# Kernel optimization log

Measured on AMD Instinct MI355X. Metric: run time of the kernel, lower is better.

Reference implementation:

```python
import jax, jax.numpy as jnp
import numpy as np

D_MODEL = 1024
NHEAD = 16
D_HEAD = D_MODEL // NHEAD


def setup_inputs() -> dict:
    key = jax.random.key(0)
    ks = jax.random.split(key, 9)
    B, S = 2, 2048
    scale = 1.0 / np.sqrt(D_MODEL)
    x = jax.random.normal(ks[0], (B, S, D_MODEL), dtype=jnp.float32)
    Wq = jax.random.normal(ks[1], (D_MODEL, D_MODEL), dtype=jnp.float32) * scale
    Wk = jax.random.normal(ks[2], (D_MODEL, D_MODEL), dtype=jnp.float32) * scale
    Wv = jax.random.normal(ks[3], (D_MODEL, D_MODEL), dtype=jnp.float32) * scale
    Wo = jax.random.normal(ks[4], (D_MODEL, D_MODEL), dtype=jnp.float32) * scale
    bq = jax.random.normal(ks[5], (D_MODEL,), dtype=jnp.float32) * 0.01
    bk = jax.random.normal(ks[6], (D_MODEL,), dtype=jnp.float32) * 0.01
    bv = jax.random.normal(ks[7], (D_MODEL,), dtype=jnp.float32) * 0.01
    bo = jax.random.normal(ks[8], (D_MODEL,), dtype=jnp.float32) * 0.01
    return {"x": x, "Wq": Wq, "bq": bq, "Wk": Wk, "bk": bk,
            "Wv": Wv, "bv": bv, "Wo": Wo, "bo": bo}


def reference(x, Wq, bq, Wk, bk, Wv, bv, Wo, bo):
    B, S, D = x.shape
    H, Dh = NHEAD, D_HEAD
    # projections; weights stored as (in, out) so y = x @ W + b
    def split_heads(t):  # [B,S,D] -> [B,H,S,Dh]
        return t.reshape(B, S, H, Dh).transpose(0, 2, 1, 3)
    q = split_heads(x @ Wq + bq)
    k = split_heads(x @ Wk + bk)
    v = split_heads(x @ Wv + bv)
    scale = 1.0 / jnp.sqrt(jnp.asarray(Dh, dtype=x.dtype))
    attn = jnp.einsum("bhqd,bhkd->bhqk", q, k) * scale  # [B,H,S,S]
    attn = jax.nn.softmax(attn, axis=-1)
    out = jnp.einsum("bhqk,bhkd->bhqd", attn, v)  # [B,H,S,Dh]
    out = out.transpose(0, 2, 1, 3).reshape(B, S, D)
    return out @ Wo + bo
```

## Files before the change

kernel.cpp:

```cpp
#include <hip/hip_runtime.h>
#include <hip/hip_bf16.h>
#include <stdint.h>
#include <stddef.h>

typedef __bf16 b16;
typedef __bf16 b16x4 __attribute__((ext_vector_type(4)));
typedef __bf16 b16x8 __attribute__((ext_vector_type(8)));
typedef float  f32x4 __attribute__((ext_vector_type(4)));

#define LOG2E 1.4426950408889634f
#define QSCALE (0.125f * LOG2E)

#if __has_builtin(__builtin_amdgcn_exp2f)
#define EXP2F(x) __builtin_amdgcn_exp2f(x)
#else
#define EXP2F(x) exp2f(x)
#endif

typedef __attribute__((address_space(1))) void gvoid;
typedef __attribute__((address_space(3))) void svoid;

__device__ __forceinline__ void async_cp16(void* lds, const void* g) {
    __builtin_amdgcn_global_load_lds((gvoid*)(void*)g, (svoid*)lds, 16, 0, 0);
}

#define SW(r) ((((r) & 7)) ^ (((r) >> 1) & 4))

__global__ __launch_bounds__(256) void k_prep(const float* __restrict__ x,
                                              const float* __restrict__ Wq,
                                              const float* __restrict__ Wk,
                                              const float* __restrict__ Wv,
                                              const float* __restrict__ Wo,
                                              b16* __restrict__ Xb,
                                              b16* __restrict__ WtQKV,
                                              b16* __restrict__ Wot) {
    const int z = blockIdx.z;
    if (z == 4) {
        const int blk = blockIdx.y * 32 + blockIdx.x;
        const float* src = x + (size_t)blk * 4096;
        b16* dst = Xb + (size_t)blk * 4096;
#pragma unroll
        for (int c = 0; c < 4; ++c) {
            const int i = c * 1024 + threadIdx.x * 4;
            float4 v = *(const float4*)(src + i);
            b16x4 o = { (b16)v.x, (b16)v.y, (b16)v.z, (b16)v.w };
            *(b16x4*)(dst + i) = o;
        }
        return;
    }
    __shared__ float t[32][33];
    const float* W = (z == 0) ? Wq : (z == 1) ? Wk : (z == 2) ? Wv : Wo;
    const int k0 = blockIdx.x * 32, n0 = blockIdx.y * 32;
    const int tr = threadIdx.x >> 3, tc4 = (threadIdx.x & 7) * 4;
    float4 v = *(const float4*)(W + (size_t)(k0 + tr) * 1024 + n0 + tc4);
    t[tr][tc4 + 0] = v.x; t[tr][tc4 + 1] = v.y;
    t[tr][tc4 + 2] = v.z; t[tr][tc4 + 3] = v.w;
    __syncthreads();
    b16* dst = (z < 3) ? (WtQKV + ((size_t)z << 20)) : Wot;
    b16x4 o = { (b16)t[tc4 + 0][tr], (b16)t[tc4 + 1][tr],
                (b16)t[tc4 + 2][tr], (b16)t[tc4 + 3][tr] };
    *(b16x4*)(dst + (size_t)(n0 + tr) * 1024 + k0 + tc4) = o;
}

__device__ __forceinline__ void gemm128_core(const b16* __restrict__ Ag,
                                             const b16* __restrict__ Bg,
                                             b16* As, b16* Bs, int tid,
                                             f32x4 acc[4][4]) {
    const int lane = tid & 63, wave = tid >> 6;
    const int wm = wave & 1, wn = wave >> 1;
    const int quad = lane >> 4, lc = lane & 15;
    const int ci0 = tid, ci1 = tid + 256;
    const b16* a0 = Ag + (ci0 >> 2) * 1024 + (ci0 & 3) * 8;
    const b16* a1 = Ag + (ci1 >> 2) * 1024 + (ci1 & 3) * 8;
    const b16* b0 = Bg + (ci0 >> 2) * 1024 + (ci0 & 3) * 8;
    const b16* b1 = Bg + (ci1 >> 2) * 1024 + (ci1 & 3) * 8;

#define GSTAGE(BUF, K0) do {                                   \
        async_cp16(As + (BUF) * 4096 + ci0 * 8, a0 + (K0));    \
        async_cp16(As + (BUF) * 4096 + ci1 * 8, a1 + (K0));    \
        async_cp16(Bs + (BUF) * 4096 + ci0 * 8, b0 + (K0));    \
        async_cp16(Bs + (BUF) * 4096 + ci1 * 8, b1 + (K0));    \
    } while (0)

#define GSTEP(BUF, SBUF, SK0, VM, DOSTAGE) do {                          \
        if (DOSTAGE) GSTAGE(SBUF, SK0);                                  \
        asm volatile("s_waitcnt vmcnt(" #VM ")" ::: "memory");           \
        __builtin_amdgcn_s_barrier();                                    \
        __builtin_amdgcn_sched_barrier(0);                               \
        b16x8 af[4], bfr[4];                                             \
        const b16* Al = As + (BUF) * 4096;                               \
        const b16* Bl = Bs + (BUF) * 4096;                               \
        _Pragma("unroll")                                                \
        for (int mt = 0; mt < 4; ++mt)                                   \
            af[mt] = *(const b16x8*)(Al + (wm * 64 + mt * 16 + lc) * 32 + quad * 8); \
        _Pragma("unroll")                                                \
        for (int nt = 0; nt < 4; ++nt)                                   \
            bfr[nt] = *(const b16x8*)(Bl + (wn * 64 + nt * 16 + lc) * 32 + quad * 8); \
        asm volatile("s_waitcnt lgkmcnt(0)" ::: "memory");               \
        __builtin_amdgcn_sched_barrier(0);                               \
        __builtin_amdgcn_s_barrier();                                    \
        __builtin_amdgcn_s_setprio(1);                                   \
        _Pragma("unroll")                                                \
        for (int mt = 0; mt < 4; ++mt)                                   \
            _Pragma("unroll")                                            \
            for (int nt = 0; nt < 4; ++nt)                               \
                acc[mt][nt] = __builtin_amdgcn_mfma_f32_16x16x32_bf16(   \
                    af[mt], bfr[nt], acc[mt][nt], 0, 0, 0);              \
        __builtin_amdgcn_s_setprio(0);                                   \
    } while (0)

    GSTAGE(0, 0);
    GSTAGE(1, 32);
    for (int i = 0; i < 10; ++i) {
        const int kb = 96 * i;
        GSTEP(0, 2, kb + 64, 8, 1);
        GSTEP(1, 0, kb + 96, 8, 1);
        GSTEP(2, 1, kb + 128, 8, 1);
    }
    GSTEP(0, 0, 0, 4, 0);
    GSTEP(1, 0, 0, 0, 0);
#undef GSTEP
#undef GSTAGE
}

__global__ __launch_bounds__(256, 3) void k_gemm_qkv(
    const b16* __restrict__ A, const b16* __restrict__ Bt,
    const float* __restrict__ bq, const float* __restrict__ bk,
    const float* __restrict__ bv,
    b16* __restrict__ Qg, b16* __restrict__ Kg, b16* __restrict__ Vtg) {
    __shared__ __align__(16) b16 LB[24576];
    b16* As = LB;
    b16* Bs = LB + 12288;
    char* Tb = (char*)LB;
    const int bm = blockIdx.x, bn = blockIdx.y;
    const int tid = threadIdx.x;
    const int lane = tid & 63, wave = tid >> 6;
    const int wm = wave & 1, wn = wave >> 1;
    const int quad = lane >> 4, lc = lane & 15;

    f32x4 acc[4][4] = {};
    gemm128_core(A + (size_t)(bm * 128) * 1024, Bt + (size_t)(bn * 128) * 1024,
                 As, Bs, tid, acc);

    const int mat = bn >> 3;
    const float* bp = (mat == 0) ? bq : (mat == 1) ? bk : bv;
    const float scl = (mat == 0) ? QSCALE : 1.0f;

#pragma unroll
    for (int nt = 0; nt < 4; ++nt) {
        const int ln = wn * 64 + nt * 16 + lc;
        const float bval = bp[(bn * 128 + ln) & 1023];
#pragma unroll
        for (int mt = 0; mt < 4; ++mt) {
            const int lm = wm * 64 + mt * 16 + quad * 4;
            if (mat == 2) {
                b16x4 o;
#pragma unroll
                for (int r = 0; r < 4; ++r) o[r] = (b16)(acc[mt][nt][r] + bval);
                const int byte = ln * 256 + (((lm >> 3) ^ (ln & 15)) << 4) + (lm & 7) * 2;
                *(b16x4*)(Tb + byte) = o;
            } else {
#pragma unroll
                for (int r = 0; r < 4; ++r) {
                    const int row = lm + r;
                    const int byte = row * 256 + (((ln >> 3) ^ (row & 15)) << 4) + (ln & 7) * 2;
                    *(b16*)(Tb + byte) = (b16)((acc[mt][nt][r] + bval) * scl);
                }
            }
        }
    }
    __syncthreads();

    const int chunk = tid & 7, hr0 = tid >> 3;
    const int b = bm >> 4;
    const int s_blk = (bm * 128) & 2047;
#pragma unroll
    for (int p = 0; p < 8; ++p) {
        const int hr = p * 32 + hr0;
        const int row = hr >> 1, half = hr & 1;
        const int c2 = (half * 8 + chunk) ^ (row & 15);
        b16x8 v = *(const b16x8*)(Tb + row * 256 + c2 * 16);
        if (mat == 2) {
            const int cm = (bn * 128 + row) & 1023;
            const int h = cm >> 6, dh = cm & 63;
            *(b16x8*)(Vtg + (size_t)((b * 16 + h) * 64 + dh) * 2048 +
                      s_blk + half * 64 + chunk * 8) = v;
        } else {
            const int s = s_blk + row;
            const int cm = (bn * 128 + half * 64 + chunk * 8) & 1023;
            const int h = cm >> 6, dh = cm & 63;
            b16* dst = (mat == 0) ? Qg : Kg;
            *(b16x8*)(dst + ((size_t)(b * 16 + h) * 2048 + s) * 64 + dh) = v;
        }
    }
}

__global__ __launch_bounds__(128, 2) void k_flash(
    const b16* __restrict__ Qg, const b16* __restrict__ Kg,
    const b16* __restrict__ Vtg, b16* __restrict__ AO) {
    __shared__ __align__(16) b16 Ks[2 * 64 * 64];
    __shared__ __align__(16) b16 Vs[2 * 64 * 64];
    __shared__ float Lred[2][64];

    const int bid = blockIdx.x;
    const int qb = bid >> 5;
    const int bh = bid & 31;

    const int tid = threadIdx.x, lane = tid & 63, wave = tid >> 6;
    const int quad = lane >> 4, lc = lane & 15;

    const b16* Kbh = Kg + (size_t)bh * 2048 * 64;
    const b16* Vbh = Vtg + (size_t)bh * 64 * 2048;

    const b16* pK[4];
    const b16* pV[4];
    int ci[4];
#pragma unroll
    for (int j = 0; j < 4; ++j) {
        ci[j] = tid + j * 128;
        const int r = ci[j] >> 3, cs = ci[j] & 7;
        const int gc = cs ^ SW(r);
        pK[j] = Kbh + r * 64 + gc * 8;
        pV[j] = Vbh + (size_t)r * 2048 + gc * 8;
    }

#define FSTAGE(BUF) do {                                       \
        _Pragma("unroll")                                      \
        for (int j = 0; j < 4; ++j) {                          \
            async_cp16(Ks + (BUF) * 4096 + ci[j] * 8, pK[j]);  \
            async_cp16(Vs + (BUF) * 4096 + ci[j] * 8, pV[j]);  \
            pK[j] += 4096; pV[j] += 64;                        \
        }                                                      \
    } while (0)

    FSTAGE(0);

    const b16* Qbase = Qg + ((size_t)bh * 2048 + qb * 128 + wave * 64) * 64;
    b16x8 qf[4][2];
#pragma unroll
    for (int qt = 0; qt < 4; ++qt)
#pragma unroll
        for (int ch = 0; ch < 2; ++ch)
            qf[qt][ch] = *(const b16x8*)(Qbase + (qt * 16 + lc) * 64 + ch * 32 + quad * 8);

    f32x4 oacc[4][4] = {};
    float lsum[4] = {0.f, 0.f, 0.f, 0.f};

    auto flash_tile = [&](const b16* Kc, const b16* Vc) {
#pragma unroll
        for (int ks = 0; ks < 2; ++ks) {
            b16x8 pf[4];
#pragma unroll
            for (int t = 0; t < 2; ++t) {
                const int krow = ks * 32 + (lc >> 2) * 8 + t * 4 + (lc & 3);
                b16x8 kf0 = *(const b16x8*)(Kc + krow * 64 + ((0 * 4 + quad) ^ SW(krow)) * 8);
                b16x8 kf1 = *(const b16x8*)(Kc + krow * 64 + ((1 * 4 + quad) ^ SW(krow)) * 8);
#pragma unroll
                for (int qt = 0; qt < 4; ++qt) {
                    f32x4 s = {};
                    s = __builtin_amdgcn_mfma_f32_16x16x32_bf16(kf0, qf[qt][0], s, 0, 0, 0);
                    s = __builtin_amdgcn_mfma_f32_16x16x32_bf16(kf1, qf[qt][1], s, 0, 0, 0);
                    float e0 = EXP2F(s[0]), e1 = EXP2F(s[1]);
                    float e2 = EXP2F(s[2]), e3 = EXP2F(s[3]);
                    lsum[qt] += (e0 + e1) + (e2 + e3);
                    pf[qt][t * 4 + 0] = (b16)e0;
                    pf[qt][t * 4 + 1] = (b16)e1;
                    pf[qt][t * 4 + 2] = (b16)e2;
                    pf[qt][t * 4 + 3] = (b16)e3;
                }
            }
            b16x8 vf[4];
#pragma unroll
            for (int dt = 0; dt < 4; ++dt) {
                const int row = dt * 16 + lc;
                vf[dt] = *(const b16x8*)(Vc + row * 64 + ((ks * 4 + quad) ^ SW(row)) * 8);
            }
            __builtin_amdgcn_s_setprio(1);
#pragma unroll
            for (int qt = 0; qt < 4; ++qt)
#pragma unroll
                for (int dt = 0; dt < 4; ++dt)
                    oacc[qt][dt] = __builtin_amdgcn_mfma_f32_16x16x32_bf16(
                        pf[qt], vf[dt], oacc[qt][dt], 0, 0, 0);
            __builtin_amdgcn_s_setprio(0);
        }
    };

    for (int kt = 0; kt < 32; kt += 2) {
        FSTAGE(1);
        asm volatile("s_waitcnt vmcnt(8)" ::: "memory");
        __builtin_amdgcn_s_barrier();
        __builtin_amdgcn_sched_barrier(0);
        flash_tile(Ks, Vs);
        __builtin_amdgcn_sched_barrier(0);
        __builtin_amdgcn_s_barrier();
        if (kt + 2 < 32) {
            FSTAGE(0);
            asm volatile("s_waitcnt vmcnt(8)" ::: "memory");
        } else {
            asm volatile("s_waitcnt vmcnt(0)" ::: "memory");
        }
        __builtin_amdgcn_s_barrier();
        __builtin_amdgcn_sched_barrier(0);
        flash_tile(Ks + 4096, Vs + 4096);
        __builtin_amdgcn_sched_barrier(0);
        __builtin_amdgcn_s_barrier();
    }
#undef FSTAGE

#pragma unroll
    for (int qt = 0; qt < 4; ++qt) {
        lsum[qt] += __shfl_xor(lsum[qt], 16, 64);
        lsum[qt] += __shfl_xor(lsum[qt], 32, 64);
    }

    if (quad == 0) {
#pragma unroll
        for (int qt = 0; qt < 4; ++qt) Lred[wave][qt * 16 + lc] = lsum[qt];
    }
    const int b = bh >> 4, h = bh & 15;
#pragma unroll
    for (int qt = 0; qt < 4; ++qt)
#pragma unroll
        for (int r = 0; r < 4; ++r) {
            const float inv = 1.0f / Lred[wave][qt * 16 + quad * 4 + r];
            const int s = qb * 128 + wave * 64 + qt * 16 + quad * 4 + r;
#pragma unroll
            for (int dt = 0; dt < 4; ++dt)
                AO[(size_t)(b * 2048 + s) * 1024 + h * 64 + dt * 16 + lc] =
                    (b16)(oacc[qt][dt][r] * inv);
        }
}

__global__ __launch_bounds__(256, 3) void k_gemm_out(
    const b16* __restrict__ A, const b16* __restrict__ Bt,
    const float* __restrict__ bo, float* __restrict__ out) {
    __shared__ __align__(16) b16 As[3 * 128 * 32];
    __shared__ __align__(16) b16 Bs[3 * 128 * 32];
    const int bm = blockIdx.x, bn = blockIdx.y;
    const int tid = threadIdx.x;
    const int lane = tid & 63, wave = tid >> 6;
    const int wm = wave & 1, wn = wave >> 1;
    const int quad = lane >> 4, lc = lane & 15;

    f32x4 acc[4][4] = {};
    gemm128_core(A + (size_t)(bm * 128) * 1024, Bt + (size_t)(bn * 128) * 1024,
                 As, Bs, tid, acc);

#pragma unroll
    for (int nt = 0; nt < 4; ++nt) {
        const int n = bn * 128 + wn * 64 + nt * 16 + lc;
        const float bval = bo[n];
#pragma unroll
        for (int mt = 0; mt < 4; ++mt) {
            const int m0 = bm * 128 + wm * 64 + mt * 16 + quad * 4;
#pragma unroll
            for (int r = 0; r < 4; ++r)
                out[(size_t)(m0 + r) * 1024 + n] = acc[mt][nt][r] + bval;
        }
    }
}

extern "C" void kernel_launch(void* const* d_in, const int* in_sizes, int n_in,
                              void* d_out, int out_size, void* d_ws, size_t ws_size,
                              hipStream_t stream) {
    const float* x  = (const float*)d_in[0];
    const float* Wq = (const float*)d_in[1];
    const float* bq = (const float*)d_in[2];
    const float* Wk = (const float*)d_in[3];
    const float* bk = (const float*)d_in[4];
    const float* Wv = (const float*)d_in[5];
    const float* bv = (const float*)d_in[6];
    const float* Wo = (const float*)d_in[7];
    const float* bo = (const float*)d_in[8];
    float* out = (float*)d_out;

    char* ws = (char*)d_ws;
    const size_t MB = 1024 * 1024;
    b16* Xb  = (b16*)(ws);
    b16* AO  = (b16*)(ws);
    b16* WtQ = (b16*)(ws + 8 * MB);
    b16* Wot = (b16*)(ws + 14 * MB);
    b16* Qg  = (b16*)(ws + 16 * MB);
    b16* Kg  = (b16*)(ws + 24 * MB);
    b16* Vtg = (b16*)(ws + 32 * MB);

    k_prep<<<dim3(32, 32, 5), 256, 0, stream>>>(x, Wq, Wk, Wv, Wo, Xb, WtQ, Wot);
    k_gemm_qkv<<<dim3(32, 24), 256, 0, stream>>>(Xb, WtQ, bq, bk, bv, Qg, Kg, Vtg);
    k_flash<<<dim3(512), 128, 0, stream>>>(Qg, Kg, Vtg, AO);
    k_gemm_out<<<dim3(32, 8), 256, 0, stream>>>(AO, Wot, bo, out);
}
```

Measured before the change: 206.6 us.

## Split flash attention across key halves with 256-thread blocks and merge kernel

The flash kernel now uses 256 threads covering 256 query rows per block, sharing each K/V tile across four waves. When workspace allows, the key range is split into two parts, each writing fp32 partial outputs and row sums. A new merge kernel adds the partials, normalizes and writes bf16. This keeps the block count the same while halving per-block work, at the cost of extra fp32 traffic and one more launch. The merge appears to rely on a fixed softmax offset rather than a per-part running max.

```diff
diff --git a/kernel.cpp b/kernel.cpp
--- a/kernel.cpp
+++ b/kernel.cpp
@@ -195,47 +195,48 @@
     }
 }
 
-__global__ __launch_bounds__(128, 2) void k_flash(
+__global__ __launch_bounds__(256, 2) void k_flash(
     const b16* __restrict__ Qg, const b16* __restrict__ Kg,
-    const b16* __restrict__ Vtg, b16* __restrict__ AO) {
+    const b16* __restrict__ Vtg,
+    float* __restrict__ Opart, float* __restrict__ lpart,
+    b16* __restrict__ AO, int ktiles, int direct, int np) {
     __shared__ __align__(16) b16 Ks[2 * 64 * 64];
     __shared__ __align__(16) b16 Vs[2 * 64 * 64];
-    __shared__ float Lred[2][64];
+    __shared__ float Lred[4][64];
 
     const int bid = blockIdx.x;
-    const int qb = bid >> 5;
-    const int bh = bid & 31;
+    const int gstride = np << 5;
+    const int qb = bid / gstride;
+    const int rem = bid - qb * gstride;
+    const int bh = rem / np;
+    const int part = rem - bh * np;
 
     const int tid = threadIdx.x, lane = tid & 63, wave = tid >> 6;
     const int quad = lane >> 4, lc = lane & 15;
 
     const b16* Kbh = Kg + (size_t)bh * 2048 * 64;
     const b16* Vbh = Vtg + (size_t)bh * 64 * 2048;
-
-    const b16* pK[4];
-    const b16* pV[4];
-    int ci[4];
-#pragma unroll
-    for (int j = 0; j < 4; ++j) {
-        ci[j] = tid + j * 128;
-        const int r = ci[j] >> 3, cs = ci[j] & 7;
-        const int gc = cs ^ SW(r);
-        pK[j] = Kbh + r * 64 + gc * 8;
-        pV[j] = Vbh + (size_t)r * 2048 + gc * 8;
-    }
-
-#define FSTAGE(BUF) do {                                       \
-        _Pragma("unroll")                                      \
-        for (int j = 0; j < 4; ++j) {                          \
-            async_cp16(Ks + (BUF) * 4096 + ci[j] * 8, pK[j]);  \
-            async_cp16(Vs + (BUF) * 4096 + ci[j] * 8, pV[j]);  \
-            pK[j] += 4096; pV[j] += 64;                        \
-        }                                                      \
+    const int kt0 = part * ktiles;
+
+    const int ci0 = tid, ci1 = tid + 256;
+    const int r0 = ci0 >> 3, gc0 = (ci0 & 7) ^ SW(r0);
+    const int r1 = ci1 >> 3, gc1 = (ci1 & 7) ^ SW(r1);
+    const b16* pK0 = Kbh + (size_t)(kt0 * 64 + r0) * 64 + gc0 * 8;
+    const b16* pK1 = Kbh + (size_t)(kt0 * 64 + r1) * 64 + gc1 * 8;
+    const b16* pV0 = Vbh + (size_t)r0 * 2048 + kt0 * 64 + gc0 * 8;
+    const b16* pV1 = Vbh + (size_t)r1 * 2048 + kt0 * 64 + gc1 * 8;
+
+#define FSTAGE(BUF) do {                                   \
+        async_cp16(Ks + (BUF) * 4096 + ci0 * 8, pK0);      \
+        async_cp16(Ks + (BUF) * 4096 + ci1 * 8, pK1);      \
+        async_cp16(Vs + (BUF) * 4096 + ci0 * 8, pV0);      \
+        async_cp16(Vs + (BUF) * 4096 + ci1 * 8, pV1);      \
+        pK0 += 4096; pK1 += 4096; pV0 += 64; pV1 += 64;    \
     } while (0)
 
     FSTAGE(0);
 
-    const b16* Qbase = Qg + ((size_t)bh * 2048 + qb * 128 + wave * 64) * 64;
+    const b16* Qbase = Qg + ((size_t)bh * 2048 + qb * 256 + wave * 64) * 64;
     b16x8 qf[4][2];
 #pragma unroll
     for (int qt = 0; qt < 4; ++qt)
@@ -286,17 +287,17 @@
         }
     };
 
-    for (int kt = 0; kt < 32; kt += 2) {
+    for (int kt = 0; kt < ktiles; kt += 2) {
         FSTAGE(1);
-        asm volatile("s_waitcnt vmcnt(8)" ::: "memory");
+        asm volatile("s_waitcnt vmcnt(4)" ::: "memory");
         __builtin_amdgcn_s_barrier();
         __builtin_amdgcn_sched_barrier(0);
         flash_tile(Ks, Vs);
         __builtin_amdgcn_sched_barrier(0);
         __builtin_amdgcn_s_barrier();
-        if (kt + 2 < 32) {
+        if (kt + 2 < ktiles) {
             FSTAGE(0);
-            asm volatile("s_waitcnt vmcnt(8)" ::: "memory");
+            asm volatile("s_waitcnt vmcnt(4)" ::: "memory");
         } else {
             asm volatile("s_waitcnt vmcnt(0)" ::: "memory");
         }
@@ -314,22 +315,58 @@
         lsum[qt] += __shfl_xor(lsum[qt], 32, 64);
     }
 
-    if (quad == 0) {
-#pragma unroll
-        for (int qt = 0; qt < 4; ++qt) Lred[wave][qt * 16 + lc] = lsum[qt];
-    }
+    if (!direct) {
+        float* Op = Opart + ((size_t)(part * 32 + bh) * 2048 + qb * 256 + wave * 64) * 64;
+#pragma unroll
+        for (int qt = 0; qt < 4; ++qt)
+#pragma unroll
+            for (int dt = 0; dt < 4; ++dt)
+#pragma unroll
+                for (int r = 0; r < 4; ++r)
+                    Op[(qt * 16 + quad * 4 + r) * 64 + dt * 16 + lc] = oacc[qt][dt][r];
+        if (quad == 0) {
+            float* lp = lpart + (size_t)(part * 32 + bh) * 2048 + qb * 256 + wave * 64;
+#pragma unroll
+            for (int qt = 0; qt < 4; ++qt) lp[qt * 16 + lc] = lsum[qt];
+        }
+    } else {
+        if (quad == 0) {
+#pragma unroll
+            for (int qt = 0; qt < 4; ++qt) Lred[wave][qt * 16 + lc] = lsum[qt];
+        }
+        const int b = bh >> 4, h = bh & 15;
+#pragma unroll
+        for (int qt = 0; qt < 4; ++qt)
+#pragma unroll
+            for (int r = 0; r < 4; ++r) {
+                const float inv = 1.0f / Lred[wave][qt * 16 + quad * 4 + r];
+                const int s = qb * 256 + wave * 64 + qt * 16 + quad * 4 + r;
+#pragma unroll
+                for (int dt = 0; dt < 4; ++dt)
+                    AO[(size_t)(b * 2048 + s) * 1024 + h * 64 + dt * 16 + lc] =
+                        (b16)(oacc[qt][dt][r] * inv);
+            }
+    }
+}
+
+__global__ __launch_bounds__(256) void k_merge(const float* __restrict__ Opart,
+                                               const float* __restrict__ lpart,
+                                               b16* __restrict__ AO, int np) {
+    const int bh = blockIdx.y;
+    const int q = blockIdx.x * 16 + (threadIdx.x >> 4);
+    const int d4 = (threadIdx.x & 15) * 4;
+    const size_t qi = (size_t)bh * 2048 + q;
+    f32x4 o = *(const f32x4*)(Opart + qi * 64 + d4);
+    float l = lpart[qi];
+    if (np == 2) {
+        o += *(const f32x4*)(Opart + (qi + (size_t)32 * 2048) * 64 + d4);
+        l += lpart[qi + (size_t)32 * 2048];
+    }
+    const float inv = 1.0f / l;
     const int b = bh >> 4, h = bh & 15;
-#pragma unroll
-    for (int qt = 0; qt < 4; ++qt)
-#pragma unroll
-        for (int r = 0; r < 4; ++r) {
-            const float inv = 1.0f / Lred[wave][qt * 16 + quad * 4 + r];
-            const int s = qb * 128 + wave * 64 + qt * 16 + quad * 4 + r;
-#pragma unroll
-            for (int dt = 0; dt < 4; ++dt)
-                AO[(size_t)(b * 2048 + s) * 1024 + h * 64 + dt * 16 + lc] =
-                    (b16)(oacc[qt][dt][r] * inv);
-        }
+    b16x4 ob = { (b16)(o[0] * inv), (b16)(o[1] * inv),
+                 (b16)(o[2] * inv), (b16)(o[3] * inv) };
+    *(b16x4*)(AO + (size_t)(b * 2048 + q) * 1024 + h * 64 + d4) = ob;
 }
 
 __global__ __launch_bounds__(256, 3) void k_gemm_out(
@@ -385,8 +422,17 @@
     b16* Kg  = (b16*)(ws + 24 * MB);
     b16* Vtg = (b16*)(ws + 32 * MB);
 
+    const size_t need2 = 40 * MB + 2 * (16 * MB) + 2 * 256 * 1024;
+    const int np = (ws_size >= need2) ? 2 : 1;
+    float* Opart = (float*)(ws + 40 * MB);
+    float* lpart = (float*)(ws + 40 * MB + (size_t)np * 16 * MB);
+    const int direct = (np == 1);
+
     k_prep<<<dim3(32, 32, 5), 256, 0, stream>>>(x, Wq, Wk, Wv, Wo, Xb, WtQ, Wot);
     k_gemm_qkv<<<dim3(32, 24), 256, 0, stream>>>(Xb, WtQ, bq, bk, bv, Qg, Kg, Vtg);
-    k_flash<<<dim3(512), 128, 0, stream>>>(Qg, Kg, Vtg, AO);
+    k_flash<<<dim3(8 * 32 * np), 256, 0, stream>>>(Qg, Kg, Vtg, Opart, lpart, AO,
+                                                   32 / np, direct, np);
+    if (!direct)
+        k_merge<<<dim3(128, 32), 256, 0, stream>>>(Opart, lpart, AO, np);
     k_gemm_out<<<dim3(32, 8), 256, 0, stream>>>(AO, Wot, bo, out);
 }
```

Measured after the change: 189.3 us. 8.4% less time.
